# Kernel tuning notes

Hardware: AMD Instinct MI355X
Metric: run time of the kernel (lower is better)

## Reference

```python
import jax, jax.numpy as jnp
import numpy as np

N_NODES = 50000
N_EDGES = 800000
HIDDEN = 128
MSG = 128


def setup_inputs() -> dict:
    key = jax.random.key(0)
    ks = jax.random.split(key, 10)
    s = 0.05
    return {
        "x": jax.random.normal(ks[0], (N_NODES, HIDDEN), jnp.float32),
        "h": jax.random.normal(ks[1], (N_NODES, HIDDEN), jnp.float32),
        "src": jax.random.randint(ks[2], (N_EDGES,), 0, N_NODES, jnp.int32),
        "dst": jax.random.randint(ks[3], (N_EDGES,), 0, N_NODES, jnp.int32),
        "W_msg": s * jax.random.normal(ks[4], (MSG, 2 * HIDDEN), jnp.float32),
        "b_msg": s * jax.random.normal(ks[5], (MSG,), jnp.float32),
        "W_ih": s * jax.random.normal(ks[6], (3 * HIDDEN, HIDDEN + MSG), jnp.float32),
        "W_hh": s * jax.random.normal(ks[7], (3 * HIDDEN, HIDDEN), jnp.float32),
        "b_ih": s * jax.random.normal(ks[8], (3 * HIDDEN,), jnp.float32),
        "b_hh": s * jax.random.normal(ks[9], (3 * HIDDEN,), jnp.float32),
    }


def reference(x, h, src, dst, W_msg, b_msg, W_ih, W_hh, b_ih, b_hh):
    N = x.shape[0]
    # --- message: linear on concat(x_src, detached h_src) -> [E, MSG]
    h_det = jax.lax.stop_gradient(h)  # h.detach() in original
    feat = jnp.concatenate([x[src], h_det[src]], axis=1)  # [E, 2H]
    m = feat @ W_msg.T + b_msg  # [E, MSG]
    # --- mean aggregation over incoming edges; isolated nodes get zeros (DGL semantics)
    msum = jax.ops.segment_sum(m, dst, num_segments=N)  # [N, MSG]
    deg = jax.ops.segment_sum(jnp.ones((src.shape[0],), m.dtype), dst, num_segments=N)
    c = msum / jnp.maximum(deg, 1.0)[:, None]
    # --- GRUCell update (PyTorch GRUCell math)
    inp = jnp.concatenate([x, c], axis=1)  # [N, H+MSG]
    gi = inp @ W_ih.T + b_ih
    gh = h @ W_hh.T + b_hh
    i_r, i_z, i_n = jnp.split(gi, 3, axis=1)
    h_r, h_z, h_n = jnp.split(gh, 3, axis=1)
    r = jax.nn.sigmoid(i_r + h_r)
    z = jax.nn.sigmoid(i_z + h_z)
    n = jnp.tanh(i_n + r * h_n)
    return (1.0 - z) * n + z * h
```

## Files before the change

### kernel.cpp

```cpp
#include <hip/hip_runtime.h>

#define H 128

typedef __attribute__((ext_vector_type(8))) short s16x8;
typedef __attribute__((ext_vector_type(2))) float f32x2;
typedef __attribute__((ext_vector_type(4))) float f32x4;

#define WAITBAR(N) asm volatile("s_waitcnt vmcnt(" #N ")\n\ts_barrier" ::: "memory")
#define BARO() asm volatile("s_barrier" ::: "memory")

__device__ __forceinline__ float bf2f(unsigned short u){
  unsigned x = ((unsigned)u) << 16;
  return __builtin_bit_cast(float, x);
}
__device__ __forceinline__ unsigned short f2bf(float f){
  unsigned u = __builtin_bit_cast(unsigned, f);
  u += 0x7fff + ((u >> 16) & 1);
  return (unsigned short)(u >> 16);
}

typedef __attribute__((address_space(1))) void gvoid;
typedef __attribute__((address_space(3))) void lvoid;
__device__ __forceinline__ void gload16(const void* g, void* l){
  __builtin_amdgcn_global_load_lds((gvoid*)(void*)g, (lvoid*)l, 16, 0, 0);
}

__global__ void pcf_kernel(const float* x, const float* h, const int* src, const int* dst,
                           const float* W_msg, const float* W_ih, const float* W_hh,
                           const float* b_ih, const float* b_hh,
                           unsigned short* xhs, unsigned char* xq, int* rc, unsigned short* ss16,
                           unsigned short* WmsgT, unsigned short* WbigT, float* biasb,
                           int nv, int E){
  int gid = blockIdx.x*256 + threadIdx.x;
  if(gid < E){
    int d = dst[gid];
    int p = atomicAdd(&rc[d], 1);
    if(p < 128) ss16[(long)d*128 + p] = (unsigned short)src[gid];
    return;
  }
  gid -= E;
  if(gid < 2*nv){
    const float* sp; int j, add;
    if(gid < nv){ sp = x; j = gid; add = 0; }
    else { sp = h; j = gid - nv; add = 128; }
    float4 v = ((const float4*)sp)[j];
    ushort4 o; o.x=f2bf(v.x); o.y=f2bf(v.y); o.z=f2bf(v.z); o.w=f2bf(v.w);
    int node = j >> 5, col = add + (j & 31)*4;
    int k = col >> 5, wc = col & 31;
    *(ushort4*)(xhs + (long)k*nv + node*32 + wc) = o;
    int r = __builtin_amdgcn_cvt_pk_fp8_f32(v.x, v.y, 0, false);
    r = __builtin_amdgcn_cvt_pk_fp8_f32(v.z, v.w, r, true);
    *(unsigned int*)(xq + (long)k*nv + node*32 + wc) = (unsigned)r;
    return;
  }
  int i = gid - 2*nv;
  const int NW = 512*384;
  if(i < NW){
    int hf = i / 98304; int r1 = i % 98304;
    int kt = r1 / 16384; int r2 = r1 % 16384;
    int row = r2 / 64;   int r3 = r2 % 64;
    int cw = r3 >> 3;    int j = r3 & 7;
    int c = cw ^ (row & 7);
    int k = kt*64 + c*8 + j;
    int rp = hf*256 + row;
    int q = rp >> 2, g = rp & 3;
    float v;
    if(g < 3){
      int orow = g*128 + q;
      v = (k < 256) ? W_ih[orow*256 + k] : W_hh[orow*128 + (k-256)];
    } else {
      v = (k < 256) ? 0.f : W_hh[(256 + q)*128 + (k-256)];
    }
    WbigT[i] = f2bf(v);
  } else if(i < NW + 128*256){
    int j2 = i - NW;
    int kt = j2 / 8192; int r2 = j2 % 8192;
    int row = r2 / 64;  int r3 = r2 % 64;
    int cw = r3 >> 3;   int j = r3 & 7;
    int c = cw ^ (row & 7);
    int k = kt*64 + c*8 + j;
    WmsgT[j2] = f2bf(W_msg[row*256 + k]);
  } else if(i < NW + 128*256 + 512){
    int r = i - NW - 128*256;
    int q = r >> 2, g = r & 3;
    biasb[r] = (g < 3) ? (b_ih[g*128+q] + b_hh[g*128+q]) : b_hh[256+q];
  }
}

__global__ void agg_kernel(const unsigned char* xq, const int* rc, const unsigned short* ss16,
                           unsigned short* Sb, int N){
  int tid = threadIdx.x;
  int group = tid >> 2, sub = tid & 3;
  int node = blockIdx.y*64 + group;
  if(node >= N) return;
  const unsigned char* base = xq + (long)blockIdx.x*(long)N*32;
  int cnt = rc[node];
  int use = (cnt < 128) ? cnt : 128;
  const long e0 = (long)node << 7;
  int co = sub*8;
  float a[8] = {0.f,0.f,0.f,0.f,0.f,0.f,0.f,0.f};
  int i = 0;
  for(; i+3 < use; i += 4){
    ushort4 idx = *(const ushort4*)(ss16 + e0 + i);
    uint2 q0 = *(const uint2*)(base + (long)idx.x*32 + co);
    uint2 q1 = *(const uint2*)(base + (long)idx.y*32 + co);
    uint2 q2 = *(const uint2*)(base + (long)idx.z*32 + co);
    uint2 q3 = *(const uint2*)(base + (long)idx.w*32 + co);
    #define ACC8(q) { \
      f32x2 l0 = __builtin_amdgcn_cvt_pk_f32_fp8((q).x, false); \
      f32x2 h0 = __builtin_amdgcn_cvt_pk_f32_fp8((q).x, true);  \
      f32x2 l1 = __builtin_amdgcn_cvt_pk_f32_fp8((q).y, false); \
      f32x2 h1 = __builtin_amdgcn_cvt_pk_f32_fp8((q).y, true);  \
      a[0]+=l0[0]; a[1]+=l0[1]; a[2]+=h0[0]; a[3]+=h0[1]; \
      a[4]+=l1[0]; a[5]+=l1[1]; a[6]+=h1[0]; a[7]+=h1[1]; }
    ACC8(q0); ACC8(q1); ACC8(q2); ACC8(q3);
  }
  for(; i < use; ++i){
    int s0 = ss16[e0 + i];
    uint2 q0 = *(const uint2*)(base + (long)s0*32 + co);
    ACC8(q0);
  }
  #undef ACC8
  float inv = (cnt > 0) ? 1.0f/(float)cnt : 0.f;
  unsigned short o[8];
  #pragma unroll
  for(int j=0;j<8;++j) o[j] = f2bf(a[j]*inv);
  *(s16x8*)(Sb + (long)node*256 + blockIdx.x*32 + co) = *(const s16x8*)o;
}

__global__ __launch_bounds__(512, 2) void fused_kernel(
    const unsigned short* xhs, const unsigned short* Sb,
    const unsigned short* WmsgT, const unsigned short* WbigT,
    const float* b_msg, const float* biasb, const int* deg,
    float* outp, int NN){
  __shared__ __align__(16) char lds[131072];
  char* W0 = lds;
  char* W1 = lds + 32768;
  char* N0 = lds + 65536;
  char* N1 = lds + 81920;
  char* ldsC = lds + 98304;
  float* ldsO = (float*)(lds + 32768);

  int tid = threadIdx.x;
  int lane = tid & 63, wv = tid >> 6;
  int l15 = lane & 15, l4 = lane >> 4;
  long nodebase = (long)blockIdx.x * 128;
  const long NV = (long)NN * 32;
  const f32x4 fz = {0.f,0.f,0.f,0.f};

  auto stageS = [&](int koff, char* dst){
    #pragma unroll
    for(int it=0; it<2; ++it){
      int slot = it*512 + tid;
      int row = slot >> 3, cw = slot & 7;
      int c = cw ^ (row & 7);
      long gr = nodebase + row; if(gr > NN-1) gr = NN-1;
      gload16(Sb + gr*256 + koff + c*8, dst + it*8192 + wv*1024);
    }
  };
  auto stageX = [&](int koff, char* dst){
    #pragma unroll
    for(int it=0; it<2; ++it){
      int slot = it*512 + tid;
      int row = slot >> 3, cw = slot & 7;
      int c = cw ^ (row & 7);
      int col = koff + c*8;
      int k = col >> 5, wc = col & 31;
      long gr = nodebase + row; if(gr > NN-1) gr = NN-1;
      gload16(xhs + (long)k*NV + gr*32 + wc, dst + it*8192 + wv*1024);
    }
  };
  auto stageW1k = [&](int kt, char* dst){
    #pragma unroll
    for(int it=0; it<2; ++it){
      int slot = it*512 + tid;
      gload16(WmsgT + kt*8192 + slot*8, dst + it*8192 + wv*1024);
    }
  };
  auto stageW3k = [&](int idx, char* dst){
    #pragma unroll
    for(int it=0; it<4; ++it){
      int slot = it*512 + tid;
      gload16(WbigT + (long)idx*16384 + slot*8, dst + it*8192 + wv*1024);
    }
  };

  int wm1 = wv >> 2, wn1 = wv & 3;
  f32x4 acc1[4][2];
  #pragma unroll
  for(int m=0;m<4;++m){ acc1[m][0]=fz; acc1[m][1]=fz; }

  auto compute1 = [&](const char* Wb, const char* Nb){
    __builtin_amdgcn_s_setprio(1);
    #pragma unroll
    for(int kk=0; kk<2; ++kk){
      s16x8 af[4], bn[2];
      #pragma unroll
      for(int m=0;m<4;++m){
        int fr = wm1*64 + m*16 + l15;
        af[m] = *(const s16x8*)(Wb + fr*128 + (((kk*4+l4) ^ (fr&7))*16));
      }
      #pragma unroll
      for(int n=0;n<2;++n){
        int nr = wn1*32 + n*16 + l15;
        bn[n] = *(const s16x8*)(Nb + nr*128 + (((kk*4+l4) ^ (nr&7))*16));
      }
      #pragma unroll
      for(int m=0;m<4;++m)
        #pragma unroll
        for(int n=0;n<2;++n)
          acc1[m][n] = __builtin_amdgcn_mfma_f32_16x16x32_bf16(af[m], bn[n], acc1[m][n], 0, 0, 0);
    }
    __builtin_amdgcn_s_setprio(0);
  };

  stageW1k(0, W0); stageS(0, N0);
  stageW1k(1, W1); stageS(64, N1);
  WAITBAR(4); compute1(W0, N0); BARO();
  stageW1k(2, W0); stageS(128, N0);
  WAITBAR(4); compute1(W1, N1); BARO();
  stageW1k(3, W1); stageS(192, N1);
  WAITBAR(4); compute1(W0, N0); BARO();
  stageW3k(0, W0); stageX(0, N0);
  WAITBAR(6); compute1(W1, N1); BARO();

  #pragma unroll
  for(int n=0;n<2;++n){
    int node_l = wn1*32 + n*16 + l15;
    long gn = nodebase + node_l; if(gn > NN-1) gn = NN-1;
    int dg = deg[gn];
    float msk = (dg > 0) ? 1.f : 0.f;
    #pragma unroll
    for(int m=0;m<4;++m){
      int ccb = wm1*64 + m*16 + l4*4;
      float4 bm = *(const float4*)(b_msg + ccb);
      ushort4 o;
      o.x = f2bf((acc1[m][n][0] + bm.x)*msk);
      o.y = f2bf((acc1[m][n][1] + bm.y)*msk);
      o.z = f2bf((acc1[m][n][2] + bm.z)*msk);
      o.w = f2bf((acc1[m][n][3] + bm.w)*msk);
      *(ushort4*)(ldsC + node_l*256 + (((ccb>>3) ^ (node_l&7))*16) + (ccb&4)*2) = o;
    }
  }
  __syncthreads();

  int wm = wv >> 1, wn = wv & 1;

  auto runHalf = [&](int hf){
    f32x4 acc3[4][4];
    #pragma unroll
    for(int m=0;m<4;++m)
      #pragma unroll
      for(int n=0;n<4;++n) acc3[m][n] = fz;

    auto computeN = [&](const char* Wb, const char* Nb){
      __builtin_amdgcn_s_setprio(1);
      #pragma unroll
      for(int kk=0; kk<2; ++kk){
        s16x8 af[4], bn[4];
        #pragma unroll
        for(int m=0;m<4;++m){
          int fr = wm*64 + m*16 + l15;
          af[m] = *(const s16x8*)(Wb + fr*128 + (((kk*4+l4) ^ (fr&7))*16));
        }
        #pragma unroll
        for(int n=0;n<4;++n){
          int nr = wn*64 + n*16 + l15;
          bn[n] = *(const s16x8*)(Nb + nr*128 + (((kk*4+l4) ^ (nr&7))*16));
        }
        #pragma unroll
        for(int m=0;m<4;++m)
          #pragma unroll
          for(int n=0;n<4;++n)
            acc3[m][n] = __builtin_amdgcn_mfma_f32_16x16x32_bf16(af[m], bn[n], acc3[m][n], 0, 0, 0);
      }
      __builtin_amdgcn_s_setprio(0);
    };
    auto computeC = [&](const char* Wb, int ktc){
      __builtin_amdgcn_s_setprio(1);
      #pragma unroll
      for(int kk=0; kk<2; ++kk){
        s16x8 af[4], bn[4];
        #pragma unroll
        for(int m=0;m<4;++m){
          int fr = wm*64 + m*16 + l15;
          af[m] = *(const s16x8*)(Wb + fr*128 + (((kk*4+l4) ^ (fr&7))*16));
        }
        #pragma unroll
        for(int n=0;n<4;++n){
          int nr = wn*64 + n*16 + l15;
          bn[n] = *(const s16x8*)(ldsC + nr*256 + (((ktc*8 + kk*4 + l4) ^ (nr&7))*16));
        }
        #pragma unroll
        for(int m=0;m<4;++m)
          #pragma unroll
          for(int n=0;n<4;++n)
            acc3[m][n] = __builtin_amdgcn_mfma_f32_16x16x32_bf16(af[m], bn[n], acc3[m][n], 0, 0, 0);
      }
      __builtin_amdgcn_s_setprio(0);
    };

    if(hf == 1) stageX(0, N0);
    stageW3k(hf*6+1, W1); stageX(64, N1);
    WAITBAR(6); computeN(W0, N0); BARO();
    stageW3k(hf*6+2, W0);
    WAITBAR(4); computeN(W1, N1); BARO();
    stageW3k(hf*6+3, W1);
    WAITBAR(4); computeC(W0, 0); BARO();
    stageW3k(hf*6+4, W0); stageX(128, N0);
    WAITBAR(6); computeC(W1, 1); BARO();
    stageW3k(hf*6+5, W1); stageX(192, N1);
    WAITBAR(6); computeN(W0, N0); BARO();
    if(hf == 0){
      stageW3k(6, W0);
      WAITBAR(4); computeN(W1, N1); BARO();
    } else {
      WAITBAR(0); computeN(W1, N1); BARO();
    }

    const char* hbuf = (hf == 0) ? N0 : N1;
    #pragma unroll
    for(int m=0;m<4;++m){
      int q = hf*64 + wm*16 + m*4 + l4;
      int ql = q & 63;
      float4 bb = *(const float4*)(biasb + q*4);
      #pragma unroll
      for(int n=0;n<4;++n){
        int node_l = wn*64 + n*16 + l15;
        unsigned short hu = *(const unsigned short*)(hbuf + node_l*128 +
                              (((ql>>3) ^ (node_l&7))*16) + (ql&7)*2);
        float hv = bf2f(hu);
        float vr  = acc3[m][n][0] + bb.x;
        float vz  = acc3[m][n][1] + bb.y;
        float vsn = acc3[m][n][2] + bb.z;
        float vhn = acc3[m][n][3] + bb.w;
        float r = 1.f/(1.f + __expf(-vr));
        float z = 1.f/(1.f + __expf(-vz));
        float narg = vsn + (r - 1.f)*vhn;
        float nn2 = 2.f/(1.f + __expf(-2.f*narg)) - 1.f;
        ldsO[node_l*64 + ql] = (1.f - z)*nn2 + z*hv;
      }
    }
    __syncthreads();

    #pragma unroll
    for(int it=0; it<4; ++it){
      int slot = it*512 + tid;
      int node_l = slot >> 4, f4 = slot & 15;
      long gn = nodebase + node_l;
      if(gn < NN){
        float4 v = *(const float4*)(ldsO + node_l*64 + f4*4);
        *(float4*)(outp + gn*128 + hf*64 + f4*4) = v;
      }
    }
    __syncthreads();
  };

  runHalf(0);
  runHalf(1);
}

extern "C" void kernel_launch(void* const* d_in, const int* in_sizes, int n_in,
                              void* d_out, int out_size, void* d_ws, size_t ws_size,
                              hipStream_t stream){
  const float* x     = (const float*)d_in[0];
  const float* h     = (const float*)d_in[1];
  const int*   src   = (const int*)d_in[2];
  const int*   dst   = (const int*)d_in[3];
  const float* W_msg = (const float*)d_in[4];
  const float* b_msg = (const float*)d_in[5];
  const float* W_ih  = (const float*)d_in[6];
  const float* W_hh  = (const float*)d_in[7];
  const float* b_ih  = (const float*)d_in[8];
  const float* b_hh  = (const float*)d_in[9];
  const int N = in_sizes[0] / H;
  const int E = in_sizes[2];
  float* out = (float*)d_out;

  char* p = (char*)d_ws;
  auto alloc = [&](size_t bytes)->char*{
    char* r = p; p += (bytes + 255) & ~(size_t)255; return r;
  };
  unsigned short* xhs   = (unsigned short*)alloc((size_t)N*256*2);
  unsigned short* Sb    = (unsigned short*)alloc((size_t)N*256*2);
  unsigned char*  xq    = (unsigned char*)alloc((size_t)N*256);
  unsigned short* WmsgT = (unsigned short*)alloc(128*256*2);
  unsigned short* WbigT = (unsigned short*)alloc(512*384*2);
  float*          biasb = (float*)alloc(512*4);
  int*            rc    = (int*)alloc((size_t)N*4);
  unsigned short* ss16  = (unsigned short*)alloc((size_t)N*128*2);

  hipMemsetAsync(rc, 0, (size_t)N*4, stream);
  int nv = N*H/4;
  const int NPREP = 512*384 + 128*256 + 512;
  long total = (long)E + 2L*nv + NPREP;
  pcf_kernel<<<(int)((total + 255)/256), 256, 0, stream>>>(
      x, h, src, dst, W_msg, W_ih, W_hh, b_ih, b_hh,
      xhs, xq, rc, ss16, WmsgT, WbigT, biasb, nv, E);

  dim3 gagg(8, (N + 63)/64);
  agg_kernel<<<gagg, 256, 0, stream>>>(xq, rc, ss16, Sb, N);

  int nblk = (N + 127)/128;
  fused_kernel<<<nblk, 512, 0, stream>>>(
      xhs, Sb, WmsgT, WbigT, b_msg, biasb, rc, out, N);
}
```

Measured before the change: 155.1 us.

## Partition edge bucketing by destination slice across block columns

Edge bucketing now runs on a 2D grid. Each of 8 block columns scans every edge but handles only those whose destination falls in its node slice, so the atomics and scattered ss16 writes for one slice stay localized, likely to the same XCD/L2 region. Each thread in the conversion and weight-prep part now handles 8 elements instead of 1. The cost is that src and dst are read 8 times over, and in exchange atomic contention and scattered writes spread across L2 partitions should drop.

```diff
diff --git a/kernel.cpp b/kernel.cpp
--- a/kernel.cpp
+++ b/kernel.cpp
@@ -25,65 +25,81 @@
   __builtin_amdgcn_global_load_lds((gvoid*)(void*)g, (lvoid*)l, 16, 0, 0);
 }
 
-__global__ void pcf_kernel(const float* x, const float* h, const int* src, const int* dst,
-                           const float* W_msg, const float* W_ih, const float* W_hh,
-                           const float* b_ih, const float* b_hh,
-                           unsigned short* xhs, unsigned char* xq, int* rc, unsigned short* ss16,
-                           unsigned short* WmsgT, unsigned short* WbigT, float* biasb,
-                           int nv, int E){
-  int gid = blockIdx.x*256 + threadIdx.x;
-  if(gid < E){
-    int d = dst[gid];
-    int p = atomicAdd(&rc[d], 1);
-    if(p < 128) ss16[(long)d*128 + p] = (unsigned short)src[gid];
+__global__ void pcfs_kernel(const float* x_, const float* h, const int* src, const int* dst,
+                            const float* W_msg, const float* W_ih, const float* W_hh,
+                            const float* b_ih, const float* b_hh,
+                            unsigned short* xhs, unsigned char* xq, int* rc, unsigned short* ss16,
+                            unsigned short* WmsgT, unsigned short* WbigT, float* biasb,
+                            int sliceSize, int YE, int nv, int E, int N){
+  int xb = blockIdx.x, y = blockIdx.y, tid = threadIdx.x;
+  if(y < YE){
+    int lo = xb*sliceSize;
+    int hi = lo + sliceSize; if(hi > N) hi = N;
+    int base = y*2048;
+    #pragma unroll
+    for(int it=0; it<8; ++it){
+      int e = base + it*256 + tid;
+      if(e < E){
+        int d = dst[e];
+        int s = src[e];
+        if(d >= lo && d < hi){
+          int p = atomicAdd(&rc[d], 1);
+          if(p < 128) ss16[(long)d*128 + p] = (unsigned short)s;
+        }
+      }
+    }
     return;
   }
-  gid -= E;
-  if(gid < 2*nv){
-    const float* sp; int j, add;
-    if(gid < nv){ sp = x; j = gid; add = 0; }
-    else { sp = h; j = gid - nv; add = 128; }
-    float4 v = ((const float4*)sp)[j];
-    ushort4 o; o.x=f2bf(v.x); o.y=f2bf(v.y); o.z=f2bf(v.z); o.w=f2bf(v.w);
-    int node = j >> 5, col = add + (j & 31)*4;
-    int k = col >> 5, wc = col & 31;
-    *(ushort4*)(xhs + (long)k*nv + node*32 + wc) = o;
-    int r = __builtin_amdgcn_cvt_pk_fp8_f32(v.x, v.y, 0, false);
-    r = __builtin_amdgcn_cvt_pk_fp8_f32(v.z, v.w, r, true);
-    *(unsigned int*)(xq + (long)k*nv + node*32 + wc) = (unsigned)r;
-    return;
-  }
-  int i = gid - 2*nv;
+  long w0 = ((long)(y - YE)*8 + xb)*2048 + tid;
   const int NW = 512*384;
-  if(i < NW){
-    int hf = i / 98304; int r1 = i % 98304;
-    int kt = r1 / 16384; int r2 = r1 % 16384;
-    int row = r2 / 64;   int r3 = r2 % 64;
-    int cw = r3 >> 3;    int j = r3 & 7;
-    int c = cw ^ (row & 7);
-    int k = kt*64 + c*8 + j;
-    int rp = hf*256 + row;
-    int q = rp >> 2, g = rp & 3;
-    float v;
-    if(g < 3){
-      int orow = g*128 + q;
-      v = (k < 256) ? W_ih[orow*256 + k] : W_hh[orow*128 + (k-256)];
-    } else {
-      v = (k < 256) ? 0.f : W_hh[(256 + q)*128 + (k-256)];
-    }
-    WbigT[i] = f2bf(v);
-  } else if(i < NW + 128*256){
-    int j2 = i - NW;
-    int kt = j2 / 8192; int r2 = j2 % 8192;
-    int row = r2 / 64;  int r3 = r2 % 64;
-    int cw = r3 >> 3;   int j = r3 & 7;
-    int c = cw ^ (row & 7);
-    int k = kt*64 + c*8 + j;
-    WmsgT[j2] = f2bf(W_msg[row*256 + k]);
-  } else if(i < NW + 128*256 + 512){
-    int r = i - NW - 128*256;
-    int q = r >> 2, g = r & 3;
-    biasb[r] = (g < 3) ? (b_ih[g*128+q] + b_hh[g*128+q]) : b_hh[256+q];
+  #pragma unroll 1
+  for(int it=0; it<8; ++it){
+    long w = w0 + (long)it*256;
+    if(w < 2L*nv){
+      const float* sp; long j; int add;
+      if(w < nv){ sp = x_; j = w; add = 0; }
+      else { sp = h; j = w - nv; add = 128; }
+      float4 v = ((const float4*)sp)[j];
+      ushort4 o; o.x=f2bf(v.x); o.y=f2bf(v.y); o.z=f2bf(v.z); o.w=f2bf(v.w);
+      int node = (int)(j >> 5), col = add + ((int)j & 31)*4;
+      int k = col >> 5, wc = col & 31;
+      *(ushort4*)(xhs + (long)k*nv + node*32 + wc) = o;
+      int r = __builtin_amdgcn_cvt_pk_fp8_f32(v.x, v.y, 0, false);
+      r = __builtin_amdgcn_cvt_pk_fp8_f32(v.z, v.w, r, true);
+      *(unsigned int*)(xq + (long)k*nv + node*32 + wc) = (unsigned)r;
+      continue;
+    }
+    long i = w - 2L*nv;
+    if(i < NW){
+      int hf = (int)(i / 98304); int r1 = (int)(i % 98304);
+      int kt = r1 / 16384; int r2 = r1 % 16384;
+      int row = r2 / 64;   int r3 = r2 % 64;
+      int cw = r3 >> 3;    int j = r3 & 7;
+      int c = cw ^ (row & 7);
+      int k = kt*64 + c*8 + j;
+      int rp = hf*256 + row;
+      int q = rp >> 2, g = rp & 3;
+      float v;
+      if(g < 3){
+        int orow = g*128 + q;
+        v = (k < 256) ? W_ih[orow*256 + k] : W_hh[orow*128 + (k-256)];
+      } else {
+        v = (k < 256) ? 0.f : W_hh[(256 + q)*128 + (k-256)];
+      }
+      WbigT[i] = f2bf(v);
+    } else if(i < NW + 128*256){
+      int j2 = (int)(i - NW);
+      int kt = j2 / 8192; int r2 = j2 % 8192;
+      int row = r2 / 64;  int r3 = r2 % 64;
+      int cw = r3 >> 3;   int j = r3 & 7;
+      int c = cw ^ (row & 7);
+      int k = kt*64 + c*8 + j;
+      WmsgT[j2] = f2bf(W_msg[row*256 + k]);
+    } else if(i < NW + 128*256 + 512){
+      int r = (int)(i - NW - 128*256);
+      int q = r >> 2, g = r & 3;
+      biasb[r] = (g < 3) ? (b_ih[g*128+q] + b_hh[g*128+q]) : b_hh[256+q];
+    }
   }
 }
 
@@ -393,10 +409,14 @@
   hipMemsetAsync(rc, 0, (size_t)N*4, stream);
   int nv = N*H/4;
   const int NPREP = 512*384 + 128*256 + 512;
-  long total = (long)E + 2L*nv + NPREP;
-  pcf_kernel<<<(int)((total + 255)/256), 256, 0, stream>>>(
+  int sliceSize = (N + 7)/8;
+  int YE = (E + 2047)/2048;
+  long convTotal = 2L*nv + NPREP;
+  int YC = (int)((convTotal + 2048L*8 - 1)/(2048L*8));
+  dim3 gpcf(8, YE + YC);
+  pcfs_kernel<<<gpcf, 256, 0, stream>>>(
       x, h, src, dst, W_msg, W_ih, W_hh, b_ih, b_hh,
-      xhs, xq, rc, ss16, WmsgT, WbigT, biasb, nv, E);
+      xhs, xq, rc, ss16, WmsgT, WbigT, biasb, sliceSize, YE, nv, E, N);
 
   dim3 gagg(8, (N + 63)/64);
   agg_kernel<<<gagg, 256, 0, stream>>>(xq, rc, ss16, Sb, N);
```

Measured after the change: 146.6 us. 5.5% less time.
